# Kernel tuning notes

Hardware: AMD Instinct MI355X
Metric: run time of the kernel (lower is better)

## Reference

```python
import jax, jax.numpy as jnp
import numpy as np

BETA = 6.0

@jax.custom_vjp
def mysign(x):
    e = jnp.exp(BETA * x)
    return ((e - 1.0) / (e + 1.0) + 1.0) / 2.0

def _mysign_fwd(x):
    return mysign(x), x

def _mysign_bwd(x, g):
    e = jnp.exp(BETA * x)
    # faithful to the custom torch backward (extra beta factor vs true gradient)
    return (BETA * (BETA * e) / jnp.square(e + 1.0) * g,)

mysign.defvjp(_mysign_fwd, _mysign_bwd)

N = 4096
E = 262144
EC = 65536
T = 512

def setup_inputs() -> dict:
    key = jax.random.key(0)
    k1, k2, k3, k4, k5 = jax.random.split(key, 5)
    edges = jax.random.randint(k1, (E, 2), 0, N, dtype=jnp.int32)
    weights = jax.random.normal(k2, (E,), dtype=jnp.float32)
    stat = jnp.ones((E,), dtype=jnp.float32)
    edges_c = jax.random.randint(k3, (EC, 2), 0, N, dtype=jnp.int32)
    grdt = jax.random.uniform(k4, (EC,), dtype=jnp.float32)
    targets = jax.random.randint(k5, (T,), 0, N, dtype=jnp.int32)
    return {"edges": edges, "weights": weights, "stat": stat,
            "edges_c": edges_c, "grdt": grdt, "targets": targets, "n": N}

def reference(edges, weights, stat, edges_c, grdt, targets, n):
    # Densify sparse COO tensors (duplicate indices sum, matching torch coalesce)
    W = jnp.zeros((n, n), weights.dtype).at[edges[:, 0], edges[:, 1]].add(weights)
    A = jnp.zeros((n, n), stat.dtype).at[edges[:, 0], edges[:, 1]].add(stat)
    B = jnp.zeros((n, n), grdt.dtype).at[edges_c[:, 0], edges_c[:, 1]].add(grdt)
    V = B * (A - 1.0) + A * W                      # [n, n]

    # Soft degrees: mysign(0) = 0.5, so zero entries each contribute 0.5
    S = mysign(jnp.abs(V))                         # [n, n]
    N_in = S.sum(axis=0)                           # [n]
    N_out = S.sum(axis=1)                          # [n]

    fair0 = jnp.ones((n,), V.dtype)
    good0 = jnp.ones((n,), V.dtype)

    # Goodness update: g[node] = sum_src Fair[src] * V[src, node]
    # (nonzero filter is a no-op here since zero V entries contribute 0)
    g = fair0 @ V                                  # [n]
    good = jnp.where(N_in != 0.0, jnp.clip(g / N_in, -1.0, 1.0), good0)

    # Fairness update: only over actual nonzero out-edges (mask matters here)
    mask = V != 0.0
    contrib = jnp.where(mask, 1.0 - jnp.abs(V - good[None, :]) / 2.0, 0.0)
    f = contrib.sum(axis=1)                        # [n]
    fair = jnp.where(N_out != 0.0, jnp.clip(f / N_out, 0.0, 1.0), fair0)

    gt = good[targets]
    gsum = jnp.sum(jnp.where(jnp.isnan(gt), 0.0, gt))
    # pack objective + updated Fair/Good state into one flat output
    return jnp.concatenate([gsum[None], fair, good])
```

## Files before the change

### kernel.cpp

```cpp
#include <hip/hip_runtime.h>
#include <math.h>

#define NN 4096
#define NPART 8
#define NCHK 128
#define GR 16
#define NGRP 256
#define SCAP 32
#define HS 2048
#define NW 16

__device__ __forceinline__ float smh(float v) {
    float e = expf(6.0f * fabsf(v));
    return 0.5f * (e - 1.0f) / (e + 1.0f);
}

__global__ __launch_bounds__(512) void split_k(
    const long* __restrict__ edges, const float* __restrict__ weights,
    const float* __restrict__ stat, const long* __restrict__ edges_c,
    const float* __restrict__ grdt, float4* __restrict__ subseg,
    int* __restrict__ scnt, int E, int EC) {
    __shared__ float4 stash[32][SCAP];
    __shared__ int cnt[32];
    const int tid = threadIdx.x;
    if (tid < 32) cnt[tid] = 0;
    __syncthreads();
    const int p = blockIdx.x & (NPART - 1);
    const int chunk = blockIdx.x >> 3;
    const int total = E + EC;
    const int csz = (total + NCHK - 1) / NCHK;
    const int lo = chunk * csz;
    const int hi = min(lo + csz, total);
    for (int i = lo + tid; i < hi; i += 512) {
        long e; int isC;
        if (i < E) { e = edges[i]; isC = 0; }
        else { e = edges_c[i - E]; isC = 1; }
        int r = (int)e;
        int c = (int)(e >> 32);
        if ((c >> 9) != p) continue;
        float4 rec;
        rec.x = __int_as_float((c << 13) | (r << 1) | isC);
        if (isC) { rec.y = grdt[i - E]; rec.z = 0.f; }
        else { rec.y = stat[i]; rec.z = weights[i]; }
        rec.w = 0.f;
        int s = (c >> 4) & 31;
        int pos = atomicAdd(&cnt[s], 1);
        if (pos < SCAP) stash[s][pos] = rec;
    }
    __syncthreads();
    for (int idx = tid; idx < 32 * SCAP; idx += 512) {
        int s = idx >> 5, i = idx & (SCAP - 1);
        if (i < cnt[s]) {
            int grp = p * 32 + s;
            subseg[((size_t)grp * NCHK + chunk) * SCAP + i] = stash[s][i];
        }
    }
    if (tid < 32) {
        int grp = p * 32 + tid;
        scnt[grp * NCHK + chunk] = min(cnt[tid], SCAP);
    }
}

__global__ __launch_bounds__(1024) void colgood_k(
    const float4* __restrict__ subseg, const int* __restrict__ scnt,
    float* __restrict__ good_buf, float* __restrict__ good_out,
    float* __restrict__ fpart, float* __restrict__ npart) {
    __shared__ int hkey[HS];
    __shared__ float hA[HS], hW[HS], hB[HS];
    __shared__ float s_f[NN], s_n[NN];
    __shared__ int s_cnt[NCHK];
    __shared__ float a1[GR][NW + 1], a2[GR][NW + 1];
    __shared__ float good_l[GR];
    const int tid = threadIdx.x;
    const int wv = tid >> 6;
    const int g = (blockIdx.x & 7) * 32 + (blockIdx.x >> 3);
    const int cb = g * GR;
    for (int i = tid; i < HS; i += 1024) {
        hkey[i] = -1; hA[i] = 0.f; hW[i] = 0.f; hB[i] = 0.f;
    }
    for (int i = tid; i < NN; i += 1024) { s_f[i] = 0.f; s_n[i] = 0.f; }
    if (tid < NCHK) s_cnt[tid] = scnt[g * NCHK + tid];
    if (tid < GR * (NW + 1)) {
        ((float*)a1)[tid] = 0.f;
        ((float*)a2)[tid] = 0.f;
    }
    __syncthreads();
    {
        const int chunk = tid & (NCHK - 1);
        const int sub = tid >> 7;
        const int n = s_cnt[chunk];
        const float4* sp = subseg + ((size_t)g * NCHK + chunk) * SCAP;
        for (int i = sub; i < n; i += 8) {
            float4 rec = sp[i];
            int ct = __float_as_int(rec.x);
            int c = ct >> 13;
            int r = (ct >> 1) & 4095;
            int key = ((c - cb) << 12) | r;
            int slot = (int)(((unsigned)key * 2654435761u) >> 21) & (HS - 1);
            while (true) {
                int prev = atomicCAS(&hkey[slot], -1, key);
                if (prev == -1 || prev == key) break;
                slot = (slot + 1) & (HS - 1);
            }
            if (ct & 1) {
                atomicAdd(&hB[slot], rec.y);
            } else {
                atomicAdd(&hA[slot], rec.y);
                atomicAdd(&hW[slot], rec.z);
            }
        }
    }
    __syncthreads();
#pragma unroll
    for (int k = 0; k < HS / 1024; ++k) {
        int s = k * 1024 + tid;
        int key = hkey[s];
        if (key != -1) {
            float a = hA[s], w = hW[s], b = hB[s];
            float v = b * (a - 1.0f) + a * w;
            float sv = smh(v);
            hA[s] = v; hW[s] = sv;
            if (v != 0.0f) {
                int d = key >> 12;
                atomicAdd(&a1[d][wv], sv);
                atomicAdd(&a2[d][wv], v);
            }
        }
    }
    __syncthreads();
    if (tid < GR) {
        float nin = 0.f, gsum = 0.f;
        for (int w2 = 0; w2 < NW; ++w2) { nin += a1[tid][w2]; gsum += a2[tid][w2]; }
        float Nin = 2048.0f + nin;
        float gd = 1.0f;
        if (Nin != 0.0f) {
            float x = gsum / Nin;
            gd = x < -1.0f ? -1.0f : (x > 1.0f ? 1.0f : x);
        }
        good_l[tid] = gd;
        good_buf[cb + tid] = gd;
        good_out[cb + tid] = gd;
    }
    __syncthreads();
#pragma unroll
    for (int k = 0; k < HS / 1024; ++k) {
        int s = k * 1024 + tid;
        int key = hkey[s];
        if (key != -1) {
            float v = hA[s];
            if (v != 0.0f) {
                int r = key & 4095;
                atomicAdd(&s_n[r], hW[s]);
                atomicAdd(&s_f[r],
                          1.0f - 0.5f * fabsf(v - good_l[key >> 12]));
            }
        }
    }
    __syncthreads();
    float* fp = fpart + (size_t)blockIdx.x * NN;
    float* np = npart + (size_t)blockIdx.x * NN;
    for (int i = tid; i < NN; i += 1024) { fp[i] = s_f[i]; np[i] = s_n[i]; }
}

__global__ __launch_bounds__(256) void reduce_k(
    const float* __restrict__ fpart, const float* __restrict__ npart,
    const float* __restrict__ good_buf, const int* __restrict__ targets,
    int T, float* __restrict__ out) {
    if (blockIdx.x < NN / GR) {
        __shared__ float sf[GR][17], sn2[GR][17];
        const int tid = threadIdx.x;
        const int rl = tid & 15, sub = tid >> 4;
        const int r = blockIdx.x * GR + rl;
        float f = 0.f, n = 0.f;
        for (int j = 0; j < 16; ++j) {
            int b = sub * 16 + j;
            f += fpart[(size_t)b * NN + r];
            n += npart[(size_t)b * NN + r];
        }
        sf[rl][sub] = f; sn2[rl][sub] = n;
        __syncthreads();
        if (tid < GR) {
            float F = 0.f, Nn = 0.f;
            for (int s2 = 0; s2 < 16; ++s2) { F += sf[tid][s2]; Nn += sn2[tid][s2]; }
            float Nout = 2048.0f + Nn;
            float fair = 1.0f;
            if (Nout != 0.0f) {
                float x = F / Nout;
                fair = x < 0.0f ? 0.0f : (x > 1.0f ? 1.0f : x);
            }
            out[1 + blockIdx.x * GR + tid] = fair;
        }
    } else {
        float s = 0.f;
        for (int i = threadIdx.x; i < T; i += 256) {
            float gt = good_buf[targets[i]];
            s += (gt == gt) ? gt : 0.0f;
        }
        for (int off = 32; off > 0; off >>= 1) s += __shfl_down(s, off, 64);
        __shared__ float lds[4];
        int lane = threadIdx.x & 63, w = threadIdx.x >> 6;
        if (lane == 0) lds[w] = s;
        __syncthreads();
        if (threadIdx.x == 0) out[0] = lds[0] + lds[1] + lds[2] + lds[3];
    }
}

extern "C" void kernel_launch(void* const* d_in, const int* in_sizes, int n_in,
                              void* d_out, int out_size, void* d_ws, size_t ws_size,
                              hipStream_t stream) {
    const long*  edges   = (const long*)d_in[0];
    const float* weights = (const float*)d_in[1];
    const float* stat    = (const float*)d_in[2];
    const long*  edges_c = (const long*)d_in[3];
    const float* grdt    = (const float*)d_in[4];
    const int*   targets = (const int*)d_in[5];
    const int E  = in_sizes[1];
    const int EC = in_sizes[4];
    const int T  = in_sizes[5];
    float* out = (float*)d_out;

    int*    scnt     = (int*)d_ws;
    float*  good_buf = (float*)(scnt + NGRP * NCHK);
    float*  fpart    = good_buf + NN;
    float*  npart    = fpart + (size_t)NGRP * NN;
    float4* subseg   = (float4*)(npart + (size_t)NGRP * NN);

    split_k<<<NPART * NCHK, 512, 0, stream>>>(
        edges, weights, stat, edges_c, grdt, subseg, scnt, E, EC);

    colgood_k<<<NGRP, 1024, 0, stream>>>(subseg, scnt, good_buf,
                                         out + 1 + NN, fpart, npart);

    reduce_k<<<NN / GR + 1, 256, 0, stream>>>(fpart, npart, good_buf,
                                              targets, T, out);
}
```

Measured before the change: 37.75 us.

## Accumulate fairness partials with per-XCD global atomics instead of per-block buffers

Each column-group block used to write full 4096-entry fairness and out-degree partial arrays, which a separate kernel then summed across 256 blocks. Now each block atomically adds its shared-memory partials into one of 8 per-XCD accumulators, which split_k zeroes, and the final kernel sums only 8 rows. This cuts global write and read traffic in exchange for heavy global atomic traffic that may contend in L2. The hash table is also doubled to lower probe collisions, at the cost of more LDS and a larger table to initialise and scan.

```diff
diff --git a/kernel.cpp b/kernel.cpp
--- a/kernel.cpp
+++ b/kernel.cpp
@@ -7,7 +7,7 @@
 #define GR 16
 #define NGRP 256
 #define SCAP 32
-#define HS 2048
+#define HS 4096
 #define NW 16
 
 __device__ __forceinline__ float smh(float v) {
@@ -19,11 +19,12 @@
     const long* __restrict__ edges, const float* __restrict__ weights,
     const float* __restrict__ stat, const long* __restrict__ edges_c,
     const float* __restrict__ grdt, float4* __restrict__ subseg,
-    int* __restrict__ scnt, int E, int EC) {
+    int* __restrict__ scnt, float* __restrict__ fAll, int E, int EC) {
     __shared__ float4 stash[32][SCAP];
     __shared__ int cnt[32];
     const int tid = threadIdx.x;
     if (tid < 32) cnt[tid] = 0;
+    if (tid < 64) fAll[blockIdx.x * 64 + tid] = 0.f;
     __syncthreads();
     const int p = blockIdx.x & (NPART - 1);
     const int chunk = blockIdx.x >> 3;
@@ -64,7 +65,7 @@
 __global__ __launch_bounds__(1024) void colgood_k(
     const float4* __restrict__ subseg, const int* __restrict__ scnt,
     float* __restrict__ good_buf, float* __restrict__ good_out,
-    float* __restrict__ fpart, float* __restrict__ npart) {
+    float* __restrict__ fAll, float* __restrict__ nAll) {
     __shared__ int hkey[HS];
     __shared__ float hA[HS], hW[HS], hB[HS];
     __shared__ float s_f[NN], s_n[NN];
@@ -73,7 +74,8 @@
     __shared__ float good_l[GR];
     const int tid = threadIdx.x;
     const int wv = tid >> 6;
-    const int g = (blockIdx.x & 7) * 32 + (blockIdx.x >> 3);
+    const int xcd = blockIdx.x & 7;
+    const int g = xcd * 32 + (blockIdx.x >> 3);
     const int cb = g * GR;
     for (int i = tid; i < HS; i += 1024) {
         hkey[i] = -1; hA[i] = 0.f; hW[i] = 0.f; hB[i] = 0.f;
@@ -96,7 +98,7 @@
             int c = ct >> 13;
             int r = (ct >> 1) & 4095;
             int key = ((c - cb) << 12) | r;
-            int slot = (int)(((unsigned)key * 2654435761u) >> 21) & (HS - 1);
+            int slot = (int)(((unsigned)key * 2654435761u) >> 20) & (HS - 1);
             while (true) {
                 int prev = atomicCAS(&hkey[slot], -1, key);
                 if (prev == -1 || prev == key) break;
@@ -157,39 +159,32 @@
         }
     }
     __syncthreads();
-    float* fp = fpart + (size_t)blockIdx.x * NN;
-    float* np = npart + (size_t)blockIdx.x * NN;
-    for (int i = tid; i < NN; i += 1024) { fp[i] = s_f[i]; np[i] = s_n[i]; }
-}
-
-__global__ __launch_bounds__(256) void reduce_k(
-    const float* __restrict__ fpart, const float* __restrict__ npart,
+    float* fx = fAll + (size_t)xcd * NN;
+    float* nx = nAll + (size_t)xcd * NN;
+    for (int i = tid; i < NN; i += 1024) {
+        atomicAdd(&fx[i], s_f[i]);
+        atomicAdd(&nx[i], s_n[i]);
+    }
+}
+
+__global__ __launch_bounds__(256) void fair_k(
+    const float* __restrict__ fAll, const float* __restrict__ nAll,
     const float* __restrict__ good_buf, const int* __restrict__ targets,
     int T, float* __restrict__ out) {
-    if (blockIdx.x < NN / GR) {
-        __shared__ float sf[GR][17], sn2[GR][17];
-        const int tid = threadIdx.x;
-        const int rl = tid & 15, sub = tid >> 4;
-        const int r = blockIdx.x * GR + rl;
-        float f = 0.f, n = 0.f;
-        for (int j = 0; j < 16; ++j) {
-            int b = sub * 16 + j;
-            f += fpart[(size_t)b * NN + r];
-            n += npart[(size_t)b * NN + r];
-        }
-        sf[rl][sub] = f; sn2[rl][sub] = n;
-        __syncthreads();
-        if (tid < GR) {
-            float F = 0.f, Nn = 0.f;
-            for (int s2 = 0; s2 < 16; ++s2) { F += sf[tid][s2]; Nn += sn2[tid][s2]; }
-            float Nout = 2048.0f + Nn;
-            float fair = 1.0f;
-            if (Nout != 0.0f) {
-                float x = F / Nout;
-                fair = x < 0.0f ? 0.0f : (x > 1.0f ? 1.0f : x);
-            }
-            out[1 + blockIdx.x * GR + tid] = fair;
-        }
+    if (blockIdx.x < NN / 256) {
+        int r = blockIdx.x * 256 + threadIdx.x;
+        float F = 0.f, Nn = 0.f;
+        for (int x = 0; x < NPART; ++x) {
+            F += fAll[(size_t)x * NN + r];
+            Nn += nAll[(size_t)x * NN + r];
+        }
+        float Nout = 2048.0f + Nn;
+        float fair = 1.0f;
+        if (Nout != 0.0f) {
+            float x = F / Nout;
+            fair = x < 0.0f ? 0.0f : (x > 1.0f ? 1.0f : x);
+        }
+        out[1 + r] = fair;
     } else {
         float s = 0.f;
         for (int i = threadIdx.x; i < T; i += 256) {
@@ -221,16 +216,16 @@
 
     int*    scnt     = (int*)d_ws;
     float*  good_buf = (float*)(scnt + NGRP * NCHK);
-    float*  fpart    = good_buf + NN;
-    float*  npart    = fpart + (size_t)NGRP * NN;
-    float4* subseg   = (float4*)(npart + (size_t)NGRP * NN);
+    float*  fAll     = good_buf + NN;
+    float*  nAll     = fAll + (size_t)NPART * NN;
+    float4* subseg   = (float4*)(nAll + (size_t)NPART * NN);
 
     split_k<<<NPART * NCHK, 512, 0, stream>>>(
-        edges, weights, stat, edges_c, grdt, subseg, scnt, E, EC);
+        edges, weights, stat, edges_c, grdt, subseg, scnt, fAll, E, EC);
 
     colgood_k<<<NGRP, 1024, 0, stream>>>(subseg, scnt, good_buf,
-                                         out + 1 + NN, fpart, npart);
-
-    reduce_k<<<NN / GR + 1, 256, 0, stream>>>(fpart, npart, good_buf,
-                                              targets, T, out);
-}
+                                         out + 1 + NN, fAll, nAll);
+
+    fair_k<<<NN / 256 + 1, 256, 0, stream>>>(fAll, nAll, good_buf,
+                                             targets, T, out);
+}
```

Result: faster. 36.98 us (-2.0%).
